# Kernel tuning notes

Measured on AMD Instinct MI355X. Metric: run time of the kernel, lower is better.

Reference implementation:

```python
import jax, jax.numpy as jnp
import numpy as np

N_NODES = 50000
N_EDGES = 800000


def gcn_conv(x, edge_index, W, b):
    """PyG GCNConv: add self-loops, symmetric deg^{-1/2} normalization,
    dense transform, scatter-add aggregation."""
    n = x.shape[0]
    src, dst = edge_index[0], edge_index[1]
    # add self-loops
    loop = jnp.arange(n, dtype=src.dtype)
    src = jnp.concatenate([src, loop])
    dst = jnp.concatenate([dst, loop])
    # degree on destination nodes (includes self-loops -> deg >= 1)
    deg = jax.ops.segment_sum(jnp.ones_like(dst, dtype=x.dtype), dst, num_segments=n)
    dinv = jax.lax.rsqrt(deg)
    norm = dinv[src] * dinv[dst]  # [E+N]
    h = x @ W                     # [N, F_out] dense GEMM
    msg = h[src] * norm[:, None]  # gather + scale, [E+N, F_out]
    out = jax.ops.segment_sum(msg, dst, num_segments=n)  # scatter-add
    return out + b


def setup_inputs() -> dict:
    key = jax.random.key(0)
    ks = jax.random.split(key, 8)
    x = jax.random.normal(ks[0], (N_NODES, 100), dtype=jnp.float32)
    edge_index = jax.random.randint(ks[1], (2, N_EDGES), 0, N_NODES, dtype=jnp.int64)
    W1 = jax.random.normal(ks[2], (100, 256), dtype=jnp.float32) * 0.1
    b1 = jnp.zeros((256,), dtype=jnp.float32)
    W2 = jax.random.normal(ks[3], (256, 128), dtype=jnp.float32) * 0.06
    b2 = jnp.zeros((128,), dtype=jnp.float32)
    Wfc = jax.random.normal(ks[4], (128, 1), dtype=jnp.float32) * 0.09
    bfc = jnp.zeros((1,), dtype=jnp.float32)
    return {"x": x, "edge_index": edge_index, "W1": W1, "b1": b1,
            "W2": W2, "b2": b2, "Wfc": Wfc, "bfc": bfc}


def reference(x, edge_index, W1, b1, W2, b2, Wfc, bfc):
    # eval mode: F.dropout with training=False is identity
    h = jax.nn.relu(gcn_conv(x, edge_index, W1, b1))
    h = jax.nn.relu(gcn_conv(h, edge_index, W2, b2))
    return h @ Wfc + bfc  # [N, 1]
```

## Files before the change

### kernel.cpp

```cpp
#include <hip/hip_runtime.h>
#include <hip/hip_bf16.h>


#define F0 100
#define F1 256
#define F2 128


__global__ void zero_i32(int* p, int n) {
    int i = blockIdx.x * blockDim.x + threadIdx.x;
    if (i < n) p[i] = 0;
}

__global__ void deg_count_i(const int* __restrict__ dst, int* deg, int e) {
    int i = blockIdx.x * blockDim.x + threadIdx.x;
    if (i < e) atomicAdd(deg + dst[i], 1);
}

__global__ void make_dinv(const int* __restrict__ deg, float* __restrict__ dinv, int n) {
    int i = blockIdx.x * blockDim.x + threadIdx.x;
    if (i < n) dinv[i] = rsqrtf((float)(deg[i] + 1));
}

__global__ __launch_bounds__(256) void scan1(const int* __restrict__ deg,
                                             int* __restrict__ excl,
                                             int* __restrict__ bsum, int n) {
    __shared__ int wsum[4];
    int i = blockIdx.x * 256 + threadIdx.x;
    int lane = threadIdx.x & 63, wid = threadIdx.x >> 6;
    int v = (i < n) ? deg[i] : 0;
    int s = v;
#pragma unroll
    for (int off = 1; off < 64; off <<= 1) {
        int t = __shfl_up(s, off, 64);
        if (lane >= off) s += t;
    }
    if (lane == 63) wsum[wid] = s;
    __syncthreads();
    int add = 0;
    for (int w = 0; w < wid; w++) add += wsum[w];
    if (i < n) excl[i] = add + s - v;
    if (threadIdx.x == 255) bsum[blockIdx.x] = add + s;
}

__global__ __launch_bounds__(256) void scan2(int* __restrict__ bsum, int nb,
                                             int* __restrict__ rowptr, int n) {
    __shared__ int wsum[4];
    int lane = threadIdx.x & 63, wid = threadIdx.x >> 6;
    int v = (threadIdx.x < nb) ? bsum[threadIdx.x] : 0;
    int s = v;
#pragma unroll
    for (int off = 1; off < 64; off <<= 1) {
        int t = __shfl_up(s, off, 64);
        if (lane >= off) s += t;
    }
    if (lane == 63) wsum[wid] = s;
    __syncthreads();
    int add = 0;
    for (int w = 0; w < wid; w++) add += wsum[w];
    if (threadIdx.x < nb) bsum[threadIdx.x] = add + s - v;
    if (threadIdx.x == 255) rowptr[n] = add + s;
}

__global__ void scan3(const int* __restrict__ excl, const int* __restrict__ bsum,
                      int* __restrict__ rowptr, int n) {
    int i = blockIdx.x * 256 + threadIdx.x;
    if (i < n) rowptr[i] = excl[i] + bsum[blockIdx.x];
}

__global__ void csr_fill(const int* __restrict__ src, const int* __restrict__ dst,
                         int* cursor, int* __restrict__ csr, int e) {
    int i = blockIdx.x * blockDim.x + threadIdx.x;
    if (i < e) {
        int pos = atomicAdd(cursor + dst[i], 1);
        csr[pos] = src[i];
    }
}


__global__ __launch_bounds__(256) void pull_f100(
        const float* __restrict__ x, const int* __restrict__ rowptr,
        const int* __restrict__ csr, const float* __restrict__ dinv,
        float* __restrict__ agg, int n) {
    int wave = threadIdx.x >> 6, lane = threadIdx.x & 63;
    int v = blockIdx.x * 4 + wave;
    if (v >= n) return;
    int beg = rowptr[v], end = rowptr[v + 1];
    float dv = dinv[v];
    int half = lane >> 5;
    int q = lane & 31;
    bool act = q < 25;
    float4 acc = {0.f, 0.f, 0.f, 0.f};

    for (int base = beg; base < end; base += 64) {
        int cnt = min(64, end - base);
        int sidx = (lane < cnt) ? csr[base + lane] : v;
        float scoef = (lane < cnt) ? dinv[sidx] : 0.f;
        int npairs = (cnt + 1) >> 1;
        int p = 0;
        for (; p + 4 <= npairs; p += 4) {
            int s0 = __shfl(sidx, 2 * p + half, 64);
            int s1 = __shfl(sidx, 2 * (p + 1) + half, 64);
            int s2 = __shfl(sidx, 2 * (p + 2) + half, 64);
            int s3 = __shfl(sidx, 2 * (p + 3) + half, 64);
            float c0 = __shfl(scoef, 2 * p + half, 64);
            float c1 = __shfl(scoef, 2 * (p + 1) + half, 64);
            float c2 = __shfl(scoef, 2 * (p + 2) + half, 64);
            float c3 = __shfl(scoef, 2 * (p + 3) + half, 64);
            if (act) {
                float4 r0 = ((const float4*)(x + (size_t)s0 * F0))[q];
                float4 r1 = ((const float4*)(x + (size_t)s1 * F0))[q];
                float4 r2 = ((const float4*)(x + (size_t)s2 * F0))[q];
                float4 r3 = ((const float4*)(x + (size_t)s3 * F0))[q];
                acc.x += c0 * r0.x + c1 * r1.x + c2 * r2.x + c3 * r3.x;
                acc.y += c0 * r0.y + c1 * r1.y + c2 * r2.y + c3 * r3.y;
                acc.z += c0 * r0.z + c1 * r1.z + c2 * r2.z + c3 * r3.z;
                acc.w += c0 * r0.w + c1 * r1.w + c2 * r2.w + c3 * r3.w;
            }
        }
        for (; p < npairs; p++) {
            int s0 = __shfl(sidx, 2 * p + half, 64);
            float c0 = __shfl(scoef, 2 * p + half, 64);
            if (act) {
                float4 r0 = ((const float4*)(x + (size_t)s0 * F0))[q];
                acc.x += c0 * r0.x;
                acc.y += c0 * r0.y;
                acc.z += c0 * r0.z;
                acc.w += c0 * r0.w;
            }
        }
    }
    float ox = __shfl_down(acc.x, 32, 64);
    float oy = __shfl_down(acc.y, 32, 64);
    float oz = __shfl_down(acc.z, 32, 64);
    float ow = __shfl_down(acc.w, 32, 64);
    if (half == 0 && act) {
        float4 hv = ((const float4*)(x + (size_t)v * F0))[q];
        float4 r;
        r.x = dv * (acc.x + ox + dv * hv.x);
        r.y = dv * (acc.y + oy + dv * hv.y);
        r.z = dv * (acc.z + oz + dv * hv.z);
        r.w = dv * (acc.w + ow + dv * hv.w);
        ((float4*)(agg + (size_t)v * F0))[q] = r;
    }
}

__global__ __launch_bounds__(256) void pull_f128_fused(
        const float* __restrict__ h2, const int* __restrict__ rowptr,
        const int* __restrict__ csr, const float* __restrict__ dinv,
        const float* __restrict__ b2, const float* __restrict__ Wfc,
        const float* __restrict__ bfc, float* __restrict__ out, int n) {
    int wave = threadIdx.x >> 6, lane = threadIdx.x & 63;
    int v = blockIdx.x * 4 + wave;
    if (v >= n) return;
    int beg = rowptr[v], end = rowptr[v + 1];
    float dv = dinv[v];
    int half = lane >> 5;
    int q = lane & 31;
    float4 acc = {0.f, 0.f, 0.f, 0.f};

    for (int base = beg; base < end; base += 64) {
        int cnt = min(64, end - base);
        int sidx = (lane < cnt) ? csr[base + lane] : v;
        float scoef = (lane < cnt) ? dinv[sidx] : 0.f;
        int npairs = (cnt + 1) >> 1;
        int p = 0;
        for (; p + 4 <= npairs; p += 4) {
            int s0 = __shfl(sidx, 2 * p + half, 64);
            int s1 = __shfl(sidx, 2 * (p + 1) + half, 64);
            int s2 = __shfl(sidx, 2 * (p + 2) + half, 64);
            int s3 = __shfl(sidx, 2 * (p + 3) + half, 64);
            float c0 = __shfl(scoef, 2 * p + half, 64);
            float c1 = __shfl(scoef, 2 * (p + 1) + half, 64);
            float c2 = __shfl(scoef, 2 * (p + 2) + half, 64);
            float c3 = __shfl(scoef, 2 * (p + 3) + half, 64);
            float4 r0 = ((const float4*)(h2 + (size_t)s0 * F2))[q];
            float4 r1 = ((const float4*)(h2 + (size_t)s1 * F2))[q];
            float4 r2 = ((const float4*)(h2 + (size_t)s2 * F2))[q];
            float4 r3 = ((const float4*)(h2 + (size_t)s3 * F2))[q];
            acc.x += c0 * r0.x + c1 * r1.x + c2 * r2.x + c3 * r3.x;
            acc.y += c0 * r0.y + c1 * r1.y + c2 * r2.y + c3 * r3.y;
            acc.z += c0 * r0.z + c1 * r1.z + c2 * r2.z + c3 * r3.z;
            acc.w += c0 * r0.w + c1 * r1.w + c2 * r2.w + c3 * r3.w;
        }
        for (; p < npairs; p++) {
            int s0 = __shfl(sidx, 2 * p + half, 64);
            float c0 = __shfl(scoef, 2 * p + half, 64);
            float4 r0 = ((const float4*)(h2 + (size_t)s0 * F2))[q];
            acc.x += c0 * r0.x;
            acc.y += c0 * r0.y;
            acc.z += c0 * r0.z;
            acc.w += c0 * r0.w;
        }
    }
    float ox = __shfl_down(acc.x, 32, 64);
    float oy = __shfl_down(acc.y, 32, 64);
    float oz = __shfl_down(acc.z, 32, 64);
    float ow = __shfl_down(acc.w, 32, 64);
    float part = 0.f;
    if (half == 0) {
        float4 hv = ((const float4*)(h2 + (size_t)v * F2))[q];
        float4 b2v = ((const float4*)b2)[q];
        float4 wv = ((const float4*)Wfc)[q];
        float t0 = dv * (acc.x + ox + dv * hv.x);
        float t1 = dv * (acc.y + oy + dv * hv.y);
        float t2 = dv * (acc.z + oz + dv * hv.z);
        float t3 = dv * (acc.w + ow + dv * hv.w);
        part = fmaxf(t0 + b2v.x, 0.f) * wv.x + fmaxf(t1 + b2v.y, 0.f) * wv.y +
               fmaxf(t2 + b2v.z, 0.f) * wv.z + fmaxf(t3 + b2v.w, 0.f) * wv.w;
        part += __shfl_down(part, 16, 64);
        part += __shfl_down(part, 8, 64);
        part += __shfl_down(part, 4, 64);
        part += __shfl_down(part, 2, 64);
        part += __shfl_down(part, 1, 64);
        if (lane == 0) out[v] = part + bfc[0];
    }
}


__global__ __launch_bounds__(256) void gemm1_tiled(
        const float* __restrict__ A, const float* __restrict__ W,
        const float* __restrict__ bias, float* __restrict__ C, int n) {
    __shared__ float As[20 * 128];
    __shared__ float Bs[20 * 128];
    int tid = threadIdx.x;
    int r0 = blockIdx.x * 128;
    int c0 = blockIdx.y * 128;
    int tc = tid & 15, tr = tid >> 4;
    float acc[8][8] = {};

    for (int k0 = 0; k0 < F0; k0 += 20) {
        if (k0) __syncthreads();
        for (int idx = tid; idx < 128 * 5; idx += 256) {
            int row = idx & 127, kq = idx >> 7;
            int gr = r0 + row;
            if (gr >= n) gr = n - 1;
            float4 v = *(const float4*)(A + (size_t)gr * F0 + k0 + 4 * kq);
            As[(4 * kq + 0) * 128 + row] = v.x;
            As[(4 * kq + 1) * 128 + row] = v.y;
            As[(4 * kq + 2) * 128 + row] = v.z;
            As[(4 * kq + 3) * 128 + row] = v.w;
        }
        for (int idx = tid; idx < 20 * 32; idx += 256) {
            int k = idx >> 5, cq = idx & 31;
            *(float4*)(Bs + k * 128 + 4 * cq) =
                *(const float4*)(W + (size_t)(k0 + k) * F1 + c0 + 4 * cq);
        }
        __syncthreads();
#pragma unroll 5
        for (int k = 0; k < 20; k++) {
            float4 a0 = *(const float4*)(As + k * 128 + 4 * tr);
            float4 a1 = *(const float4*)(As + k * 128 + 64 + 4 * tr);
            float4 b0 = *(const float4*)(Bs + k * 128 + 4 * tc);
            float4 b1 = *(const float4*)(Bs + k * 128 + 64 + 4 * tc);
            float av[8] = {a0.x, a0.y, a0.z, a0.w, a1.x, a1.y, a1.z, a1.w};
            float bv[8] = {b0.x, b0.y, b0.z, b0.w, b1.x, b1.y, b1.z, b1.w};
#pragma unroll
            for (int i = 0; i < 8; i++)
#pragma unroll
                for (int j = 0; j < 8; j++) acc[i][j] += av[i] * bv[j];
        }
    }
    float4 bb0 = *(const float4*)(bias + c0 + 4 * tc);
    float4 bb1 = *(const float4*)(bias + c0 + 64 + 4 * tc);
    float bv[8] = {bb0.x, bb0.y, bb0.z, bb0.w, bb1.x, bb1.y, bb1.z, bb1.w};
#pragma unroll
    for (int i = 0; i < 8; i++) {
        int row = (i < 4) ? (4 * tr + i) : (64 + 4 * tr + i - 4);
        int gr = r0 + row;
        if (gr < n) {
            float4 o0, o1;
            o0.x = fmaxf(acc[i][0] + bv[0], 0.f);
            o0.y = fmaxf(acc[i][1] + bv[1], 0.f);
            o0.z = fmaxf(acc[i][2] + bv[2], 0.f);
            o0.w = fmaxf(acc[i][3] + bv[3], 0.f);
            o1.x = fmaxf(acc[i][4] + bv[4], 0.f);
            o1.y = fmaxf(acc[i][5] + bv[5], 0.f);
            o1.z = fmaxf(acc[i][6] + bv[6], 0.f);
            o1.w = fmaxf(acc[i][7] + bv[7], 0.f);
            *(float4*)(C + (size_t)gr * F1 + c0 + 4 * tc) = o0;
            *(float4*)(C + (size_t)gr * F1 + c0 + 64 + 4 * tc) = o1;
        }
    }
}

__global__ __launch_bounds__(256) void gemm2_tiled(
        const float* __restrict__ A, const float* __restrict__ W,
        float* __restrict__ C, int n) {
    __shared__ float As[32 * 128];
    __shared__ float Bs[32 * 128];
    int tid = threadIdx.x;
    int r0 = blockIdx.x * 128;
    int tc = tid & 15, tr = tid >> 4;
    float acc[8][8] = {};

    for (int k0 = 0; k0 < F1; k0 += 32) {
        if (k0) __syncthreads();
        for (int idx = tid; idx < 128 * 8; idx += 256) {
            int row = idx & 127, kq = idx >> 7;
            int gr = r0 + row;
            if (gr >= n) gr = n - 1;
            float4 v = *(const float4*)(A + (size_t)gr * F1 + k0 + 4 * kq);
            As[(4 * kq + 0) * 128 + row] = v.x;
            As[(4 * kq + 1) * 128 + row] = v.y;
            As[(4 * kq + 2) * 128 + row] = v.z;
            As[(4 * kq + 3) * 128 + row] = v.w;
        }
        for (int idx = tid; idx < 32 * 32; idx += 256) {
            int k = idx >> 5, cq = idx & 31;
            *(float4*)(Bs + k * 128 + 4 * cq) =
                *(const float4*)(W + (size_t)(k0 + k) * F2 + 4 * cq);
        }
        __syncthreads();
#pragma unroll 4
        for (int k = 0; k < 32; k++) {
            float4 a0 = *(const float4*)(As + k * 128 + 4 * tr);
            float4 a1 = *(const float4*)(As + k * 128 + 64 + 4 * tr);
            float4 b0 = *(const float4*)(Bs + k * 128 + 4 * tc);
            float4 b1 = *(const float4*)(Bs + k * 128 + 64 + 4 * tc);
            float av[8] = {a0.x, a0.y, a0.z, a0.w, a1.x, a1.y, a1.z, a1.w};
            float bv[8] = {b0.x, b0.y, b0.z, b0.w, b1.x, b1.y, b1.z, b1.w};
#pragma unroll
            for (int i = 0; i < 8; i++)
#pragma unroll
                for (int j = 0; j < 8; j++) acc[i][j] += av[i] * bv[j];
        }
    }
#pragma unroll
    for (int i = 0; i < 8; i++) {
        int row = (i < 4) ? (4 * tr + i) : (64 + 4 * tr + i - 4);
        int gr = r0 + row;
        if (gr < n) {
            float4 o0 = {acc[i][0], acc[i][1], acc[i][2], acc[i][3]};
            float4 o1 = {acc[i][4], acc[i][5], acc[i][6], acc[i][7]};
            *(float4*)(C + (size_t)gr * F2 + 4 * tc) = o0;
            *(float4*)(C + (size_t)gr * F2 + 64 + 4 * tc) = o1;
        }
    }
}


static inline size_t align16(size_t x) { return (x + 3) & ~(size_t)3; }

extern "C" void kernel_launch(void* const* d_in, const int* in_sizes, int n_in,
                              void* d_out, int out_size, void* d_ws, size_t ws_size,
                              hipStream_t stream) {
    const float* x   = (const float*)d_in[0];
    const int*   ei  = (const int*)d_in[1];
    const float* W1  = (const float*)d_in[2];
    const float* b1  = (const float*)d_in[3];
    const float* W2  = (const float*)d_in[4];
    const float* b2  = (const float*)d_in[5];
    const float* Wfc = (const float*)d_in[6];
    const float* bfc = (const float*)d_in[7];
    float* out = (float*)d_out;

    const int n = in_sizes[0] / F0;
    const int e = in_sizes[1] / 2;
    const int* src = ei;
    const int* dst = ei + e;

    char* wsb = (char*)d_ws;
    size_t off = 0;
    int* deg    = (int*)(wsb + 4 * off); off = align16(off + n);
    int* excl   = (int*)(wsb + 4 * off); off = align16(off + n);
    int* bsum   = (int*)(wsb + 4 * off); off = align16(off + 256);
    int* rowptr = (int*)(wsb + 4 * off); off = align16(off + n + 1);
    int* cursor = (int*)(wsb + 4 * off); off = align16(off + n);
    int* csr    = (int*)(wsb + 4 * off); off = align16(off + e);
    float* dinv = (float*)(wsb + 4 * off); off = align16(off + n);
    float* aggX = (float*)(wsb + 4 * off); off = align16(off + (size_t)n * F0);
    float* a1   = (float*)(wsb + 4 * off); off = align16(off + (size_t)n * F1);
    float* h2   = (float*)(wsb + 4 * off); off = align16(off + (size_t)n * F2);

    const int B = 256;
    const int nb = (n + B - 1) / B;
    const int rblocks = (n + 127) / 128;

    zero_i32<<<nb, B, 0, stream>>>(deg, n);
    deg_count_i<<<(e + B - 1) / B, B, 0, stream>>>(dst, deg, e);
    make_dinv<<<nb, B, 0, stream>>>(deg, dinv, n);
    scan1<<<nb, B, 0, stream>>>(deg, excl, bsum, n);
    scan2<<<1, B, 0, stream>>>(bsum, nb, rowptr, n);
    scan3<<<nb, B, 0, stream>>>(excl, bsum, rowptr, n);
    hipMemcpyAsync(cursor, rowptr, (size_t)n * 4, hipMemcpyDeviceToDevice, stream);
    csr_fill<<<(e + B - 1) / B, B, 0, stream>>>(src, dst, cursor, csr, e);

    pull_f100<<<(n + 3) / 4, 256, 0, stream>>>(x, rowptr, csr, dinv, aggX, n);
    gemm1_tiled<<<dim3(rblocks, F1 / 128), 256, 0, stream>>>(aggX, W1, b1, a1, n);

    gemm2_tiled<<<rblocks, 256, 0, stream>>>(a1, W2, h2, n);
    pull_f128_fused<<<(n + 3) / 4, 256, 0, stream>>>(h2, rowptr, csr, dinv,
                                                     b2, Wfc, bfc, out, n);
}
```

Before: 390.0 us.

## Fuse CSR construction into a single cooperative kernel with grid syncs

Replaces the seven CSR-building launches plus a device memcpy (zero, degree count, dinv, three-phase scan, cursor copy, fill) with one cooperative kernel of 1024 blocks that uses grid.sync between phases. The aim is to remove per-launch overhead and inter-kernel gaps in this small preprocessing stage, and it also drops the excl buffer. In exchange it relies on cooperative launch residency and uses grid-stride loops with fewer threads for the atomic phases.

```diff
diff --git a/kernel.cpp b/kernel.cpp
--- a/kernel.cpp
+++ b/kernel.cpp
@@ -1,78 +1,79 @@
 #include <hip/hip_runtime.h>
 #include <hip/hip_bf16.h>
+#include <hip/hip_cooperative_groups.h>
+
+namespace cg = cooperative_groups;
 
 
 #define F0 100
 #define F1 256
 #define F2 128
 
-
-__global__ void zero_i32(int* p, int n) {
-    int i = blockIdx.x * blockDim.x + threadIdx.x;
-    if (i < n) p[i] = 0;
-}
-
-__global__ void deg_count_i(const int* __restrict__ dst, int* deg, int e) {
-    int i = blockIdx.x * blockDim.x + threadIdx.x;
-    if (i < e) atomicAdd(deg + dst[i], 1);
-}
-
-__global__ void make_dinv(const int* __restrict__ deg, float* __restrict__ dinv, int n) {
-    int i = blockIdx.x * blockDim.x + threadIdx.x;
-    if (i < n) dinv[i] = rsqrtf((float)(deg[i] + 1));
-}
-
-__global__ __launch_bounds__(256) void scan1(const int* __restrict__ deg,
-                                             int* __restrict__ excl,
-                                             int* __restrict__ bsum, int n) {
+__global__ __launch_bounds__(256) void csr_coop(
+        const int* __restrict__ src, const int* __restrict__ dst,
+        int* __restrict__ deg, int* __restrict__ bsum,
+        int* __restrict__ rowptr, int* __restrict__ cursor,
+        int* __restrict__ csr, float* __restrict__ dinv, int n, int e) {
+    cg::grid_group grid = cg::this_grid();
+    const int tid = threadIdx.x;
+    const int gsz = gridDim.x * 256;
+    const int gtid = blockIdx.x * 256 + tid;
+    const int lane = tid & 63, wid = tid >> 6;
     __shared__ int wsum[4];
-    int i = blockIdx.x * 256 + threadIdx.x;
-    int lane = threadIdx.x & 63, wid = threadIdx.x >> 6;
-    int v = (i < n) ? deg[i] : 0;
-    int s = v;
-#pragma unroll
-    for (int off = 1; off < 64; off <<= 1) {
-        int t = __shfl_up(s, off, 64);
-        if (lane >= off) s += t;
-    }
-    if (lane == 63) wsum[wid] = s;
-    __syncthreads();
-    int add = 0;
-    for (int w = 0; w < wid; w++) add += wsum[w];
-    if (i < n) excl[i] = add + s - v;
-    if (threadIdx.x == 255) bsum[blockIdx.x] = add + s;
-}
-
-__global__ __launch_bounds__(256) void scan2(int* __restrict__ bsum, int nb,
-                                             int* __restrict__ rowptr, int n) {
-    __shared__ int wsum[4];
-    int lane = threadIdx.x & 63, wid = threadIdx.x >> 6;
-    int v = (threadIdx.x < nb) ? bsum[threadIdx.x] : 0;
-    int s = v;
-#pragma unroll
-    for (int off = 1; off < 64; off <<= 1) {
-        int t = __shfl_up(s, off, 64);
-        if (lane >= off) s += t;
-    }
-    if (lane == 63) wsum[wid] = s;
-    __syncthreads();
-    int add = 0;
-    for (int w = 0; w < wid; w++) add += wsum[w];
-    if (threadIdx.x < nb) bsum[threadIdx.x] = add + s - v;
-    if (threadIdx.x == 255) rowptr[n] = add + s;
-}
-
-__global__ void scan3(const int* __restrict__ excl, const int* __restrict__ bsum,
-                      int* __restrict__ rowptr, int n) {
-    int i = blockIdx.x * 256 + threadIdx.x;
-    if (i < n) rowptr[i] = excl[i] + bsum[blockIdx.x];
-}
-
-__global__ void csr_fill(const int* __restrict__ src, const int* __restrict__ dst,
-                         int* cursor, int* __restrict__ csr, int e) {
-    int i = blockIdx.x * blockDim.x + threadIdx.x;
-    if (i < e) {
-        int pos = atomicAdd(cursor + dst[i], 1);
+
+    for (int i = gtid; i < n; i += gsz) deg[i] = 0;
+    grid.sync();
+
+    for (int i = gtid; i < e; i += gsz) atomicAdd(&deg[dst[i]], 1);
+    grid.sync();
+
+    const int nb = (n + 255) / 256;
+    for (int b = blockIdx.x; b < nb; b += gridDim.x) {
+        int i = b * 256 + tid;
+        int v = (i < n) ? deg[i] : 0;
+        if (i < n) dinv[i] = rsqrtf((float)(v + 1));
+        int s = v;
+#pragma unroll
+        for (int off = 1; off < 64; off <<= 1) {
+            int t = __shfl_up(s, off, 64);
+            if (lane >= off) s += t;
+        }
+        if (lane == 63) wsum[wid] = s;
+        __syncthreads();
+        int add = 0;
+        for (int w = 0; w < wid; w++) add += wsum[w];
+        if (i < n) rowptr[i] = add + s - v;
+        if (tid == 255) bsum[b] = add + s;
+        __syncthreads();
+    }
+    grid.sync();
+
+    if (blockIdx.x == 0) {
+        int v = (tid < nb) ? bsum[tid] : 0;
+        int s = v;
+#pragma unroll
+        for (int off = 1; off < 64; off <<= 1) {
+            int t = __shfl_up(s, off, 64);
+            if (lane >= off) s += t;
+        }
+        if (lane == 63) wsum[wid] = s;
+        __syncthreads();
+        int add = 0;
+        for (int w = 0; w < wid; w++) add += wsum[w];
+        if (tid < nb) bsum[tid] = add + s - v;
+    }
+    grid.sync();
+
+    for (int i = gtid; i < n; i += gsz) {
+        int r = rowptr[i] + bsum[i >> 8];
+        rowptr[i] = r;
+        cursor[i] = r;
+    }
+    if (gtid == 0) rowptr[n] = e;
+    grid.sync();
+
+    for (int i = gtid; i < e; i += gsz) {
+        int pos = atomicAdd(&cursor[dst[i]], 1);
         csr[pos] = src[i];
     }
 }
@@ -355,15 +356,14 @@
     const float* bfc = (const float*)d_in[7];
     float* out = (float*)d_out;
 
-    const int n = in_sizes[0] / F0;
-    const int e = in_sizes[1] / 2;
+    int n = in_sizes[0] / F0;
+    int e = in_sizes[1] / 2;
     const int* src = ei;
     const int* dst = ei + e;
 
     char* wsb = (char*)d_ws;
     size_t off = 0;
     int* deg    = (int*)(wsb + 4 * off); off = align16(off + n);
-    int* excl   = (int*)(wsb + 4 * off); off = align16(off + n);
     int* bsum   = (int*)(wsb + 4 * off); off = align16(off + 256);
     int* rowptr = (int*)(wsb + 4 * off); off = align16(off + n + 1);
     int* cursor = (int*)(wsb + 4 * off); off = align16(off + n);
@@ -373,18 +373,15 @@
     float* a1   = (float*)(wsb + 4 * off); off = align16(off + (size_t)n * F1);
     float* h2   = (float*)(wsb + 4 * off); off = align16(off + (size_t)n * F2);
 
-    const int B = 256;
-    const int nb = (n + B - 1) / B;
     const int rblocks = (n + 127) / 128;
 
-    zero_i32<<<nb, B, 0, stream>>>(deg, n);
-    deg_count_i<<<(e + B - 1) / B, B, 0, stream>>>(dst, deg, e);
-    make_dinv<<<nb, B, 0, stream>>>(deg, dinv, n);
-    scan1<<<nb, B, 0, stream>>>(deg, excl, bsum, n);
-    scan2<<<1, B, 0, stream>>>(bsum, nb, rowptr, n);
-    scan3<<<nb, B, 0, stream>>>(excl, bsum, rowptr, n);
-    hipMemcpyAsync(cursor, rowptr, (size_t)n * 4, hipMemcpyDeviceToDevice, stream);
-    csr_fill<<<(e + B - 1) / B, B, 0, stream>>>(src, dst, cursor, csr, e);
+    {
+        void* args[] = {(void*)&src, (void*)&dst, (void*)&deg, (void*)&bsum,
+                        (void*)&rowptr, (void*)&cursor, (void*)&csr,
+                        (void*)&dinv, (void*)&n, (void*)&e};
+        hipLaunchCooperativeKernel((void*)csr_coop, dim3(1024), dim3(256),
+                                   args, 0, stream);
+    }
 
     pull_f100<<<(n + 3) / 4, 256, 0, stream>>>(x, rowptr, csr, dinv, aggX, n);
     gemm1_tiled<<<dim3(rblocks, F1 / 128), 256, 0, stream>>>(aggX, W1, b1, a1, n);
```

New measurement: 858.2 us. +120.1%, slower.
